# Performance work log

Measured on AMD Instinct MI355X. Metric: run time of the kernel, lower is better.

Reference implementation:

```python
import jax, jax.numpy as jnp
import numpy as np

B, N, H, C = 8, 128, 768, 5


def setup_inputs() -> dict:
    key = jax.random.key(0)
    k0, k1, k2, k3 = jax.random.split(key, 4)
    h = jax.random.normal(k0, (B, N, H), dtype=jnp.float32)
    # torch nn.Linear(4H, H): out = x @ W.T + b; we store Wcat = W.T with shape [4H, H]
    Wcat = jax.random.normal(k1, (4 * H, H), dtype=jnp.float32) * 0.02
    bW = jnp.zeros((H,), dtype=jnp.float32)
    h_hat = jax.random.normal(k2, (H,), dtype=jnp.float32)
    Wout = jax.random.normal(k3, (H, C), dtype=jnp.float32) * 0.02
    bout = jnp.zeros((C,), dtype=jnp.float32)
    return {"h": h, "Wcat": Wcat, "bW": bW, "h_hat": h_hat, "Wout": Wout, "bout": bout}


def reference(h, Wcat, bW, h_hat, Wout, bout):
    n = h.shape[1]
    W1, W2, W3, W4 = jnp.split(Wcat, 4, axis=0)  # each [H, H]
    # span order matches the torch double loop: i in range(N), j in range(i, N)
    ii, jj = jnp.triu_indices(n)  # P = n(n+1)/2
    # cat([hi,hj,hi-hj,hi*hj]) @ Wcat == hi@(W1+W3) + hj@(W2-W3) + (hi*hj)@W4
    A = jnp.einsum('bnh,hk->bnk', h, W1 + W3)   # [B, N, H]
    Bm = jnp.einsum('bnh,hk->bnk', h, W2 - W3)  # [B, N, H]
    prod = h[:, ii, :] * h[:, jj, :]            # [B, P, H]
    spans = jnp.tanh(A[:, ii, :] + Bm[:, jj, :]
                     + jnp.einsum('bph,hk->bpk', prod, W4) + bW)  # [B, P, H]
    # InterpretationLayer: attention pooling over spans
    alpha = jax.nn.softmax(jnp.einsum('bph,h->bp', spans, h_hat), axis=1)
    h_tilde = jnp.einsum('bp,bph->bh', alpha, spans)  # [B, H]
    logits = h_tilde @ Wout + bout                    # [B, C]
    return jax.nn.log_softmax(logits, axis=1)
```

## Files before the change

### kernel.cpp

```cpp
#include <hip/hip_runtime.h>
#include <hip/hip_bf16.h>


#define B_ 8
#define N_ 128
#define H_ 768
#define C_ 5
#define P_ 8256
#define TP 64
#define NBLK 129
#define NSTEP 24

typedef short bf16x8 __attribute__((ext_vector_type(8)));
typedef float f32x4 __attribute__((ext_vector_type(4)));

__device__ __forceinline__ float bf2f(unsigned short u){
  union { unsigned u; float f; } v; v.u = ((unsigned)u) << 16; return v.f;
}
__device__ __forceinline__ unsigned short f2bf(float f){
  union { float f; unsigned u; } v; v.f = f;
  unsigned r = v.u + 0x7FFFu + ((v.u >> 16) & 1u);
  return (unsigned short)(r >> 16);
}
__device__ __forceinline__ float tanh_fast(float x){
  float e = __expf(2.f * x);
  return 1.f - 2.f / (e + 1.f);
}
__device__ __forceinline__ bf16x8 prodpack(bf16x8 x, bf16x8 y){
  union { bf16x8 v; unsigned u[4]; } o;
  #pragma unroll
  for (int e2 = 0; e2 < 4; e2++){
    float p0 = bf2f((unsigned short)x[e2*2])   * bf2f((unsigned short)y[e2*2]);
    float p1 = bf2f((unsigned short)x[e2*2+1]) * bf2f((unsigned short)y[e2*2+1]);
    unsigned pk;
    asm volatile("v_cvt_pk_bf16_f32 %0, %1, %2" : "=v"(pk) : "v"(p0), "v"(p1));
    o.u[e2] = pk;
  }
  return o.v;
}
__device__ __forceinline__ int lds_off(int row, int k){
  return row * (H_ * 2) + ((k * 2) ^ ((row & 15) << 4));
}


#define PH_BLKS 3072
#define PW_BLKS 288
#define PR_BLKS 33

__global__ void prep(const float* __restrict__ h, const float* __restrict__ Wcat,
                     unsigned short* __restrict__ hb,
                     unsigned short* __restrict__ Wsum,
                     unsigned short* __restrict__ Wdif,
                     unsigned short* __restrict__ W4s,
                     int* __restrict__ ii, int* __restrict__ jj){
  const int bid = blockIdx.x;
  if (bid < PH_BLKS){
    int idx = bid * 256 + threadIdx.x;
    hb[idx] = f2bf(h[idx]);
  } else if (bid < PH_BLKS + PW_BLKS){
    int idx = (bid - PH_BLKS) * 256 + threadIdx.x;
    int o = idx / H_, col = idx % H_;
    bf16x8 vs, vd, v4;
    #pragma unroll
    for (int e = 0; e < 8; e++){
      int hrow = o * 8 + e;
      float w1 = Wcat[hrow * H_ + col];
      float w2 = Wcat[(H_ + hrow) * H_ + col];
      float w3 = Wcat[(2 * H_ + hrow) * H_ + col];
      float w4 = Wcat[(3 * H_ + hrow) * H_ + col];
      vs[e] = (short)f2bf(w1 + w3);
      vd[e] = (short)f2bf(w2 - w3);
      v4[e] = (short)f2bf(w4);
    }
    int pbase = (o * H_ + col) * 8;
    *(bf16x8*)(Wsum + pbase) = vs;
    *(bf16x8*)(Wdif + pbase) = vd;
    *(bf16x8*)(W4s + pbase)  = v4;
  } else {
    int p = (bid - PH_BLKS - PW_BLKS) * 256 + threadIdx.x;
    if (p < P_){
      int i = 0, off = 0;
      while (off + (N_ - i) <= p){ off += (N_ - i); i++; }
      ii[p] = i; jj[p] = i + (p - off);
    }
  }
}


__global__ __launch_bounds__(512, 4) void coef_gemm(
    const unsigned short* __restrict__ hb,
    const unsigned short* __restrict__ Wsum,
    const unsigned short* __restrict__ Wdif,
    const float* __restrict__ bW,
    float* __restrict__ Acoef, float* __restrict__ Bcoef){
  const int sel = blockIdx.y;
  const unsigned short* Wp = sel ? Wdif : Wsum;
  float* out = sel ? Bcoef : Acoef;
  const int growb = blockIdx.x * 16;

  __shared__ char As[16 * H_ * 2];

  const int tid = threadIdx.x;
  {
    int r = tid >> 5;
    int c = tid & 31;
    const unsigned short* src = hb + (growb + r) * H_;
    #pragma unroll
    for (int kk = 0; kk < 3; kk++){
      int k = kk * 256 + c * 8;
      bf16x8 v = *(const bf16x8*)(src + k);
      *(bf16x8*)(As + lds_off(r, k)) = v;
    }
  }
  __syncthreads();

  const int lane = tid & 63;
  const int wn = tid >> 6;
  const int hi = lane >> 4;
  const int l15 = lane & 15;
  const int colbase = wn * 96 + l15;

  f32x4 acc[6] = {};

  const bf16x8* wp = (const bf16x8*)Wp + hi * H_ + colbase;
  bf16x8 bc0 = wp[0], bc1 = wp[16], bc2 = wp[32], bc3 = wp[48], bc4 = wp[64], bc5 = wp[80];
  wp += 4 * H_;
  for (int step = 0; step < 24; ++step){
    bf16x8 bn0 = wp[0], bn1 = wp[16], bn2 = wp[32], bn3 = wp[48], bn4 = wp[64], bn5 = wp[80];
    wp += 4 * H_;
    bf16x8 a = *(const bf16x8*)(As + lds_off(l15, step * 32 + hi * 8));
    acc[0] = __builtin_amdgcn_mfma_f32_16x16x32_bf16(a, bc0, acc[0], 0, 0, 0);
    acc[1] = __builtin_amdgcn_mfma_f32_16x16x32_bf16(a, bc1, acc[1], 0, 0, 0);
    acc[2] = __builtin_amdgcn_mfma_f32_16x16x32_bf16(a, bc2, acc[2], 0, 0, 0);
    acc[3] = __builtin_amdgcn_mfma_f32_16x16x32_bf16(a, bc3, acc[3], 0, 0, 0);
    acc[4] = __builtin_amdgcn_mfma_f32_16x16x32_bf16(a, bc4, acc[4], 0, 0, 0);
    acc[5] = __builtin_amdgcn_mfma_f32_16x16x32_bf16(a, bc5, acc[5], 0, 0, 0);
    bc0 = bn0; bc1 = bn1; bc2 = bn2; bc3 = bn3; bc4 = bn4; bc5 = bn5;
  }

  #pragma unroll
  for (int ni = 0; ni < 6; ni++){
    int col = colbase + ni * 16;
    float bw = (sel == 0) ? bW[col] : 0.f;
    #pragma unroll
    for (int r = 0; r < 4; r++){
      int grow = growb + hi * 4 + r;
      out[grow * H_ + col] = acc[ni][r] + bw;
    }
  }
}


__global__ __launch_bounds__(1024, 4)
void spans_fused(
    const unsigned short* __restrict__ hb,
    const float* __restrict__ Acoef,
    const float* __restrict__ Bcoef,
    const unsigned short* __restrict__ W4s,
    const float* __restrict__ hhat,
    const int* __restrict__ ii,
    const int* __restrict__ jj,
    float* __restrict__ pm, float* __restrict__ pl, float* __restrict__ pacc){
  __shared__ char As[TP * H_ * 2];
  __shared__ int iis[TP], jjs[TP];
  __shared__ float sbuf[16][TP];
  __shared__ float wbuf[TP];

  const int bid = blockIdx.x;
  const int b = bid / NBLK;
  const int p0 = (bid % NBLK) * TP;
  const int tid = threadIdx.x;

  if (tid < TP){ iis[tid] = ii[p0 + tid]; jjs[tid] = jj[p0 + tid]; }
  __syncthreads();

  {
    int r = tid >> 4;
    int c = tid & 15;
    const unsigned short* hp = hb + (b * N_ + iis[r]) * H_;
    const unsigned short* hq = hb + (b * N_ + jjs[r]) * H_;
    #pragma unroll
    for (int kk = 0; kk < 6; kk++){
      int k = kk * 128 + c * 8;
      bf16x8 va = *(const bf16x8*)(hp + k);
      bf16x8 vb = *(const bf16x8*)(hq + k);
      *(bf16x8*)(As + lds_off(r, k)) = prodpack(va, vb);
    }
  }

  const int lane = tid & 63;
  const int wave = tid >> 6;
  const int hi = lane >> 4;
  const int l15 = lane & 15;
  const int colbase = wave * 48 + l15;

  f32x4 acc[4][3];
  #pragma unroll
  for (int mi = 0; mi < 4; mi++){
    #pragma unroll
    for (int r = 0; r < 4; r++){
      int rowl = mi * 16 + hi * 4 + r;
      const float* ap = Acoef + (b * N_ + iis[rowl]) * H_ + colbase;
      const float* bp = Bcoef + (b * N_ + jjs[rowl]) * H_ + colbase;
      #pragma unroll
      for (int ni = 0; ni < 3; ni++)
        acc[mi][ni][r] = ap[ni * 16] + bp[ni * 16];
    }
  }

  const bf16x8* wp = (const bf16x8*)W4s + hi * H_ + colbase;
  bf16x8 bs[3][3];
  #pragma unroll
  for (int s = 0; s < 2; s++)
    #pragma unroll
    for (int ni = 0; ni < 3; ni++)
      bs[s][ni] = wp[s * 4 * H_ + ni * 16];

  __syncthreads();

  #pragma unroll
  for (int t = 0; t < NSTEP; ++t){
    if (t + 2 < NSTEP){
      #pragma unroll
      for (int ni = 0; ni < 3; ni++)
        bs[(t + 2) % 3][ni] = wp[(t + 2) * 4 * H_ + ni * 16];
    }
    const int kb = t * 32 + hi * 8;
    bf16x8 a0 = *(const bf16x8*)(As + lds_off(     l15, kb));
    bf16x8 a1 = *(const bf16x8*)(As + lds_off(16 + l15, kb));
    bf16x8 a2 = *(const bf16x8*)(As + lds_off(32 + l15, kb));
    bf16x8 a3 = *(const bf16x8*)(As + lds_off(48 + l15, kb));
    #pragma unroll
    for (int ni = 0; ni < 3; ni++){
      bf16x8 bfr = bs[t % 3][ni];
      acc[0][ni] = __builtin_amdgcn_mfma_f32_16x16x32_bf16(a0, bfr, acc[0][ni], 0, 0, 0);
      acc[1][ni] = __builtin_amdgcn_mfma_f32_16x16x32_bf16(a1, bfr, acc[1][ni], 0, 0, 0);
      acc[2][ni] = __builtin_amdgcn_mfma_f32_16x16x32_bf16(a2, bfr, acc[2][ni], 0, 0, 0);
      acc[3][ni] = __builtin_amdgcn_mfma_f32_16x16x32_bf16(a3, bfr, acc[3][ni], 0, 0, 0);
    }
  }

  float sc[4][4];
  #pragma unroll
  for (int mi = 0; mi < 4; mi++)
    #pragma unroll
    for (int r = 0; r < 4; r++) sc[mi][r] = 0.f;

  #pragma unroll
  for (int ni = 0; ni < 3; ni++){
    float hh = hhat[colbase + ni * 16];
    #pragma unroll
    for (int mi = 0; mi < 4; mi++){
      #pragma unroll
      for (int r = 0; r < 4; r++){
        float s = tanh_fast(acc[mi][ni][r]);
        acc[mi][ni][r] = s;
        sc[mi][r] += s * hh;
      }
    }
  }
  #pragma unroll
  for (int mi = 0; mi < 4; mi++)
    #pragma unroll
    for (int r = 0; r < 4; r++){
      float v = sc[mi][r];
      v += __shfl_xor(v, 1); v += __shfl_xor(v, 2);
      v += __shfl_xor(v, 4); v += __shfl_xor(v, 8);
      sc[mi][r] = v;
    }
  if (l15 == 0){
    #pragma unroll
    for (int mi = 0; mi < 4; mi++)
      #pragma unroll
      for (int r = 0; r < 4; r++)
        sbuf[wave][mi * 16 + hi * 4 + r] = sc[mi][r];
  }
  __syncthreads();

  if (tid < TP){
    float s = 0.f;
    #pragma unroll
    for (int w = 0; w < 16; w++) s += sbuf[w][tid];
    float m = s;
    #pragma unroll
    for (int off = 1; off < 64; off <<= 1) m = fmaxf(m, __shfl_xor(m, off));
    float w = __expf(s - m);
    float l = w;
    #pragma unroll
    for (int off = 1; off < 64; off <<= 1) l += __shfl_xor(l, off);
    wbuf[tid] = w;
    if (tid == 0){ pm[bid] = m; pl[bid] = l; }
  }
  __syncthreads();

  #pragma unroll
  for (int ni = 0; ni < 3; ni++){
    float wa = 0.f;
    #pragma unroll
    for (int mi = 0; mi < 4; mi++)
      #pragma unroll
      for (int r = 0; r < 4; r++){
        int rowl = mi * 16 + hi * 4 + r;
        wa += wbuf[rowl] * acc[mi][ni][r];
      }
    wa += __shfl_xor(wa, 16);
    wa += __shfl_xor(wa, 32);
    if (lane < 16) pacc[bid * H_ + colbase + ni * 16] = wa;
  }
}


__global__ void merge1(
    const float* __restrict__ pm, const float* __restrict__ pl,
    const float* __restrict__ pacc, float* __restrict__ htg){
  __shared__ float ebuf[NBLK];
  __shared__ float Msh, invLsh;
  __shared__ float part[128];
  const int b = blockIdx.x;
  const int ch = blockIdx.y;
  const int tid = threadIdx.x;

  if (tid < 64){
    float m = -3.4e38f;
    for (int t = tid; t < NBLK; t += 64) m = fmaxf(m, pm[b * NBLK + t]);
    #pragma unroll
    for (int off = 1; off < 64; off <<= 1) m = fmaxf(m, __shfl_xor(m, off));
    float l = 0.f;
    for (int t = tid; t < NBLK; t += 64) l += pl[b * NBLK + t] * __expf(pm[b * NBLK + t] - m);
    #pragma unroll
    for (int off = 1; off < 64; off <<= 1) l += __shfl_xor(l, off);
    if (tid == 0){ Msh = m; invLsh = 1.f / l; }
  }
  __syncthreads();
  if (tid < NBLK) ebuf[tid] = __expf(pm[b * NBLK + tid] - Msh);
  __syncthreads();
  const int col = ch * 128 + (tid & 127);
  const int half = tid >> 7;
  float a = 0.f;
  for (int t = half; t < NBLK; t += 2) a += pacc[(b * NBLK + t) * H_ + col] * ebuf[t];
  if (half) part[tid & 127] = a;
  __syncthreads();
  if (!half) htg[b * H_ + col] = (a + part[tid]) * invLsh;
}


__global__ void merge2(
    const float* __restrict__ htg,
    const float* __restrict__ Wout, const float* __restrict__ bout,
    float* __restrict__ outp){
  const int b = blockIdx.x;
  const int lane = threadIdx.x;
  float a[C_] = {};
  for (int k = lane; k < H_; k += 64){
    float hv = htg[b * H_ + k];
    #pragma unroll
    for (int c = 0; c < C_; c++) a[c] += hv * Wout[k * C_ + c];
  }
  #pragma unroll
  for (int c = 0; c < C_; c++){
    #pragma unroll
    for (int off = 1; off < 64; off <<= 1) a[c] += __shfl_xor(a[c], off);
  }
  if (lane == 0){
    float lg[C_];
    #pragma unroll
    for (int c = 0; c < C_; c++) lg[c] = a[c] + bout[c];
    float mx = lg[0];
    #pragma unroll
    for (int c = 1; c < C_; c++) mx = fmaxf(mx, lg[c]);
    float s = 0.f;
    #pragma unroll
    for (int c = 0; c < C_; c++) s += __expf(lg[c] - mx);
    float ls = __logf(s) + mx;
    #pragma unroll
    for (int c = 0; c < C_; c++) outp[b * C_ + c] = lg[c] - ls;
  }
}


extern "C" void kernel_launch(void* const* d_in, const int* in_sizes, int n_in,
                              void* d_out, int out_size, void* d_ws, size_t ws_size,
                              hipStream_t stream){
  const float* h    = (const float*)d_in[0];
  const float* Wcat = (const float*)d_in[1];
  const float* bW   = (const float*)d_in[2];
  const float* hhat = (const float*)d_in[3];
  const float* Wout = (const float*)d_in[4];
  const float* bout = (const float*)d_in[5];
  float* outp = (float*)d_out;

  unsigned short* hb   = (unsigned short*)d_ws;
  unsigned short* Wsum = hb + 786432;
  unsigned short* Wdif = Wsum + 589824;
  unsigned short* W4s  = Wdif + 589824;
  float* Acoef = (float*)(W4s + 589824);
  float* Bcoef = Acoef + 786432;
  int* iiA = (int*)(Bcoef + 786432);
  int* jjA = iiA + P_;
  float* pm = (float*)(jjA + P_);
  float* pl = pm + (B_ * NBLK);
  float* pacc = pl + (B_ * NBLK);
  float* htg  = pacc + (B_ * NBLK * H_);

  prep<<<PH_BLKS + PW_BLKS + PR_BLKS, 256, 0, stream>>>(h, Wcat, hb, Wsum, Wdif, W4s, iiA, jjA);
  coef_gemm<<<dim3(64, 2), 512, 0, stream>>>(hb, Wsum, Wdif, bW, Acoef, Bcoef);
  spans_fused<<<B_ * NBLK, 1024, 0, stream>>>(hb, Acoef, Bcoef, W4s, hhat, iiA, jjA, pm, pl, pacc);
  merge1<<<dim3(B_, 6), 256, 0, stream>>>(pm, pl, pacc, htg);
  merge2<<<B_, 64, 0, stream>>>(htg, Wout, bout, outp);
}
```

Baseline: 174.8 us.

## Store A/B coefficients as bf16, interleave batches in grid, deepen W4 prefetch, raise MFMA priority

The A and B coefficient tensors written by coef_gemm and gathered by spans_fused are now stored as bf16 instead of fp32, halving that traffic. The block index is remapped so consecutive blocks cover different batches of the same span tile. The W4 register prefetch ring grows from three to four stages, and s_setprio wraps the MFMA burst. Rounding A and B to bf16 before tanh adds a little numerical error, and the deeper ring uses more registers.

```diff
diff --git a/kernel.cpp b/kernel.cpp
--- a/kernel.cpp
+++ b/kernel.cpp
@@ -92,10 +92,10 @@
     const unsigned short* __restrict__ Wsum,
     const unsigned short* __restrict__ Wdif,
     const float* __restrict__ bW,
-    float* __restrict__ Acoef, float* __restrict__ Bcoef){
+    unsigned short* __restrict__ Acoef, unsigned short* __restrict__ Bcoef){
   const int sel = blockIdx.y;
   const unsigned short* Wp = sel ? Wdif : Wsum;
-  float* out = sel ? Bcoef : Acoef;
+  unsigned short* out = sel ? Bcoef : Acoef;
   const int growb = blockIdx.x * 16;
 
   __shared__ char As[16 * H_ * 2];
@@ -145,7 +145,7 @@
     #pragma unroll
     for (int r = 0; r < 4; r++){
       int grow = growb + hi * 4 + r;
-      out[grow * H_ + col] = acc[ni][r] + bw;
+      out[grow * H_ + col] = f2bf(acc[ni][r] + bw);
     }
   }
 }
@@ -154,8 +154,8 @@
 __global__ __launch_bounds__(1024, 4)
 void spans_fused(
     const unsigned short* __restrict__ hb,
-    const float* __restrict__ Acoef,
-    const float* __restrict__ Bcoef,
+    const unsigned short* __restrict__ Acoef,
+    const unsigned short* __restrict__ Bcoef,
     const unsigned short* __restrict__ W4s,
     const float* __restrict__ hhat,
     const int* __restrict__ ii,
@@ -166,9 +166,11 @@
   __shared__ float sbuf[16][TP];
   __shared__ float wbuf[TP];
 
-  const int bid = blockIdx.x;
-  const int b = bid / NBLK;
-  const int p0 = (bid % NBLK) * TP;
+  const int bidraw = blockIdx.x;
+  const int b = bidraw & 7;
+  const int tile = bidraw >> 3;
+  const int bid = b * NBLK + tile;
+  const int p0 = tile * TP;
   const int tid = threadIdx.x;
 
   if (tid < TP){ iis[tid] = ii[p0 + tid]; jjs[tid] = jj[p0 + tid]; }
@@ -200,18 +202,18 @@
     #pragma unroll
     for (int r = 0; r < 4; r++){
       int rowl = mi * 16 + hi * 4 + r;
-      const float* ap = Acoef + (b * N_ + iis[rowl]) * H_ + colbase;
-      const float* bp = Bcoef + (b * N_ + jjs[rowl]) * H_ + colbase;
+      const unsigned short* ap = Acoef + (b * N_ + iis[rowl]) * H_ + colbase;
+      const unsigned short* bp = Bcoef + (b * N_ + jjs[rowl]) * H_ + colbase;
       #pragma unroll
       for (int ni = 0; ni < 3; ni++)
-        acc[mi][ni][r] = ap[ni * 16] + bp[ni * 16];
+        acc[mi][ni][r] = bf2f(ap[ni * 16]) + bf2f(bp[ni * 16]);
     }
   }
 
   const bf16x8* wp = (const bf16x8*)W4s + hi * H_ + colbase;
-  bf16x8 bs[3][3];
-  #pragma unroll
-  for (int s = 0; s < 2; s++)
+  bf16x8 bs[4][3];
+  #pragma unroll
+  for (int s = 0; s < 3; s++)
     #pragma unroll
     for (int ni = 0; ni < 3; ni++)
       bs[s][ni] = wp[s * 4 * H_ + ni * 16];
@@ -220,24 +222,26 @@
 
   #pragma unroll
   for (int t = 0; t < NSTEP; ++t){
-    if (t + 2 < NSTEP){
+    if (t + 3 < NSTEP){
       #pragma unroll
       for (int ni = 0; ni < 3; ni++)
-        bs[(t + 2) % 3][ni] = wp[(t + 2) * 4 * H_ + ni * 16];
+        bs[(t + 3) & 3][ni] = wp[(t + 3) * 4 * H_ + ni * 16];
     }
     const int kb = t * 32 + hi * 8;
     bf16x8 a0 = *(const bf16x8*)(As + lds_off(     l15, kb));
     bf16x8 a1 = *(const bf16x8*)(As + lds_off(16 + l15, kb));
     bf16x8 a2 = *(const bf16x8*)(As + lds_off(32 + l15, kb));
     bf16x8 a3 = *(const bf16x8*)(As + lds_off(48 + l15, kb));
+    __builtin_amdgcn_s_setprio(1);
     #pragma unroll
     for (int ni = 0; ni < 3; ni++){
-      bf16x8 bfr = bs[t % 3][ni];
+      bf16x8 bfr = bs[t & 3][ni];
       acc[0][ni] = __builtin_amdgcn_mfma_f32_16x16x32_bf16(a0, bfr, acc[0][ni], 0, 0, 0);
       acc[1][ni] = __builtin_amdgcn_mfma_f32_16x16x32_bf16(a1, bfr, acc[1][ni], 0, 0, 0);
       acc[2][ni] = __builtin_amdgcn_mfma_f32_16x16x32_bf16(a2, bfr, acc[2][ni], 0, 0, 0);
       acc[3][ni] = __builtin_amdgcn_mfma_f32_16x16x32_bf16(a3, bfr, acc[3][ni], 0, 0, 0);
     }
+    __builtin_amdgcn_s_setprio(0);
   }
 
   float sc[4][4];
@@ -393,8 +397,8 @@
   unsigned short* Wsum = hb + 786432;
   unsigned short* Wdif = Wsum + 589824;
   unsigned short* W4s  = Wdif + 589824;
-  float* Acoef = (float*)(W4s + 589824);
-  float* Bcoef = Acoef + 786432;
+  unsigned short* Acoef = W4s + 589824;
+  unsigned short* Bcoef = Acoef + 786432;
   int* iiA = (int*)(Bcoef + 786432);
   int* jjA = iiA + P_;
   float* pm = (float*)(jjA + P_);
```

New measurement: 229.0 us. 1.31x slower.
